# Optimization experiments

Measured on AMD Instinct MI355X. Metric: run time of the kernel, lower is better.

The kernel has to match this reference:

```python
import jax, jax.numpy as jnp
import numpy as np

EMB_SIZE = 768
NUM_HEADS = 8


def setup_inputs() -> dict:
    key = jax.random.key(0)
    ks = jax.random.split(key, 6)
    B, N, E = 8, 1024, EMB_SIZE
    return {
        "x": jax.random.normal(ks[0], (B, N, E), dtype=jnp.float32),
        "relative_pos": jax.random.normal(ks[1], (NUM_HEADS, N, N), dtype=jnp.float32),
        "qkv_w": jax.random.normal(ks[2], (2 * E, E), dtype=jnp.float32) * 0.02,
        "qkv_b": jax.random.normal(ks[3], (2 * E,), dtype=jnp.float32) * 0.02,
        "val_w": jax.random.normal(ks[4], (E, E), dtype=jnp.float32) * 0.02,
        "val_b": jax.random.normal(ks[5], (E,), dtype=jnp.float32) * 0.02,
    }


def reference(x, relative_pos, qkv_w, qkv_b, val_w, val_b):
    B, N, E = x.shape
    H = NUM_HEADS
    D = E // H
    # qkv projection: [B, N, 2E]; last dim layout is (h, d, qk) per einops rearrange
    qkv = (x @ qkv_w.T + qkv_b).reshape(B, N, H, D, 2)
    q = jnp.transpose(qkv[..., 0], (0, 2, 1, 3))  # [B, H, N, D]
    k = jnp.transpose(qkv[..., 1], (0, 2, 1, 3))  # [B, H, N, D]
    scale = E ** 0.5  # original divides by sqrt(emb_size), not sqrt(d_head)
    energy = jnp.einsum('bhqd,bhkd->bhqk', q, k) / scale  # [B, H, N, N]
    # relative_pos [H, N, N] broadcasts over batch
    energy = jax.nn.softmax(energy + relative_pos, axis=-1)
    values = x @ val_w.T + val_b  # [B, N, E]
    return values, energy
```

## Files before the change

### kernel.cpp

```cpp
#include <hip/hip_runtime.h>
#include <hip/hip_bf16.h>

#define EMB 768
#define NH 8
#define DH 96
#define BATCH 8
#define SEQ 1024
#define M_TOT (BATCH * SEQ)
#define NCOLS (3 * EMB)

typedef float f32x4 __attribute__((ext_vector_type(4)));
typedef __bf16 bf16x8 __attribute__((ext_vector_type(8)));

__device__ __forceinline__ unsigned short f2bf_bits(float f) {
  __hip_bfloat16 b = __float2bfloat16(f);
  return *reinterpret_cast<unsigned short*>(&b);
}

__device__ __forceinline__ void gload_lds16(const void* g, void* l) {
  __builtin_amdgcn_global_load_lds(
      (__attribute__((address_space(1))) void*)(g),
      (__attribute__((address_space(3))) void*)(l), 16, 0, 0);
}

__global__ void prep_x_kernel(const float* __restrict__ x, __hip_bfloat16* __restrict__ xb) {
  const int n4 = M_TOT * EMB / 4;
  int i = blockIdx.x * blockDim.x + threadIdx.x;
  if (i < n4) {
    f32x4 v = reinterpret_cast<const f32x4*>(x)[i];
    ushort4 o;
    o.x = f2bf_bits(v[0]);
    o.y = f2bf_bits(v[1]);
    o.z = f2bf_bits(v[2]);
    o.w = f2bf_bits(v[3]);
    reinterpret_cast<ushort4*>(xb)[i] = o;
  }
}

__global__ void prep_w_kernel(const float* __restrict__ qkv_w, const float* __restrict__ qkv_b,
                              const float* __restrict__ val_w, const float* __restrict__ val_b,
                              __hip_bfloat16* __restrict__ Wall, float* __restrict__ bias) {
  const float inv_s = 0.03608439182435161f;
  int idx = blockIdx.x * 256 + threadIdx.x;
  if (idx >= NCOLS * EMB) return;
  int r = idx / EMB;
  int c = idx - r * EMB;
  float v;
  if (r < EMB) {
    int h = r / DH, d = r - h * DH;
    int src = h * 192 + 2 * d;
    v = qkv_w[(size_t)src * EMB + c] * inv_s;
    if (c == 0) bias[r] = qkv_b[src] * inv_s;
  } else if (r < 2 * EMB) {
    int r2 = r - EMB;
    int h = r2 / DH, d = r2 - h * DH;
    int src = h * 192 + 2 * d + 1;
    v = qkv_w[(size_t)src * EMB + c];
    if (c == 0) bias[r] = qkv_b[src];
  } else {
    int r3 = r - 2 * EMB;
    v = val_w[(size_t)r3 * EMB + c];
    if (c == 0) bias[r] = val_b[r3];
  }
  Wall[idx] = __float2bfloat16(v);
}

__global__ __launch_bounds__(256) void gemm_kernel(
    const __hip_bfloat16* __restrict__ xb, const __hip_bfloat16* __restrict__ Wall,
    const float* __restrict__ bias, __hip_bfloat16* __restrict__ qhead,
    __hip_bfloat16* __restrict__ khead, float* __restrict__ vout) {
  __shared__ __hip_bfloat16 As[128 * 32];
  __shared__ __hip_bfloat16 Bs[128 * 32];
  const int tid = threadIdx.x;
  const int w = tid >> 6, l = tid & 63;
  const int m0 = blockIdx.x * 128;
  const int n0 = blockIdx.y * 128;
  const int wr = w >> 1, wc = w & 1;

  f32x4 acc[4][4] = {};

  const int sr0 = (w * 2 + 0) * 16 + (l >> 2);
  const int sr1 = (w * 2 + 1) * 16 + (l >> 2);
  const int sc = (l & 3) * 8;

  for (int kt = 0; kt < EMB / 32; ++kt) {
    const int k0 = kt * 32;
    gload_lds16(xb + (size_t)(m0 + sr0) * EMB + k0 + sc, (void*)(As + (w * 2 + 0) * 512));
    gload_lds16(xb + (size_t)(m0 + sr1) * EMB + k0 + sc, (void*)(As + (w * 2 + 1) * 512));
    gload_lds16(Wall + (size_t)(n0 + sr0) * EMB + k0 + sc, (void*)(Bs + (w * 2 + 0) * 512));
    gload_lds16(Wall + (size_t)(n0 + sr1) * EMB + k0 + sc, (void*)(Bs + (w * 2 + 1) * 512));
    __syncthreads();

    bf16x8 af[4], bfr[4];
#pragma unroll
    for (int t = 0; t < 4; ++t) {
      af[t] = *reinterpret_cast<const bf16x8*>(As + (wr * 64 + t * 16 + (l & 15)) * 32 + (l >> 4) * 8);
      bfr[t] = *reinterpret_cast<const bf16x8*>(Bs + (wc * 64 + t * 16 + (l & 15)) * 32 + (l >> 4) * 8);
    }
#pragma unroll
    for (int i = 0; i < 4; ++i)
#pragma unroll
      for (int j = 0; j < 4; ++j)
        acc[i][j] = __builtin_amdgcn_mfma_f32_16x16x32_bf16(af[i], bfr[j], acc[i][j], 0, 0, 0);
    __syncthreads();
  }

  const int rowbase = m0 + wr * 64;
  const int colbase = n0 + wc * 64;
#pragma unroll
  for (int j = 0; j < 4; ++j) {
    const int n = colbase + j * 16 + (l & 15);
    const float bb = bias[n];
#pragma unroll
    for (int i = 0; i < 4; ++i) {
#pragma unroll
      for (int q = 0; q < 4; ++q) {
        const int m = rowbase + i * 16 + (l >> 4) * 4 + q;
        const float v = acc[i][j][q] + bb;
        if (n0 >= 2 * EMB) {
          vout[(size_t)m * EMB + (n - 2 * EMB)] = v;
        } else {
          const int nn = (n0 >= EMB) ? (n - EMB) : n;
          const int hh = nn / DH, dd = nn - hh * DH;
          const size_t off = ((size_t)((m >> 10) * NH + hh) * SEQ + (m & 1023)) * DH + dd;
          if (n0 >= EMB) khead[off] = __float2bfloat16(v);
          else qhead[off] = __float2bfloat16(v);
        }
      }
    }
  }
}

__global__ __launch_bounds__(512, 4) void attn_kernel(
    const __hip_bfloat16* __restrict__ qhead, const __hip_bfloat16* __restrict__ khead,
    const float* __restrict__ rel, float* __restrict__ eout) {
  __shared__ alignas(16) char KS[49152];
  __shared__ float redm[16][8];
  __shared__ float reds[16][8];

  const int t = threadIdx.x;
  const int w = t >> 6, l = t & 63;
  const int lr = l >> 4, lc = l & 15;
  const int flat = blockIdx.x;
  const int u = flat >> 6;
  const int b = (flat >> 3) & 7;
  const int g = u * 8 + (flat & 7);
  const int h = g >> 6;
  const int rb = g & 63;
  const int row0 = rb * 16;

  const __hip_bfloat16* qsrc = qhead + ((size_t)(b * NH + h) * SEQ + row0 + lc) * DH;
  bf16x8 qf[3];
#pragma unroll
  for (int kc = 0; kc < 3; ++kc)
    qf[kc] = *reinterpret_cast<const bf16x8*>(qsrc + kc * 32 + lr * 8);

  const __hip_bfloat16* ksrc =
      khead + (size_t)(b * NH + h) * SEQ * DH + (size_t)w * 16 * DH;
  char* kdst = KS + w * 6144;

#define STAGE_K(c, buf)                                                             \
  {                                                                                 \
    const __hip_bfloat16* s_ = ksrc + (size_t)(c) * 12288 + (size_t)l * 8;          \
    gload_lds16(s_, kdst + (buf) * 3072);                                           \
    gload_lds16(s_ + 512, kdst + (buf) * 3072 + 1024);                              \
    gload_lds16(s_ + 1024, kdst + (buf) * 3072 + 2048);                             \
  }

  STAGE_K(0, 0)

  const float* relsrc = rel + ((size_t)h * SEQ + row0 + lc) * SEQ + w * 16 + lr * 4;
  f32x4 acc[8];

#pragma unroll
  for (int c = 0; c < 8; ++c) {
    f32x4 relv = *reinterpret_cast<const f32x4*>(relsrc + c * 128);
    if (c < 7) STAGE_K(c + 1, (c + 1) & 1)
    if (c < 7) {
      asm volatile("s_waitcnt vmcnt(4)" ::: "memory");
    } else {
      asm volatile("s_waitcnt vmcnt(1)" ::: "memory");
    }
    __builtin_amdgcn_sched_barrier(0);
    const __hip_bfloat16* kp =
        reinterpret_cast<const __hip_bfloat16*>(kdst + (c & 1) * 3072) + lc * DH;
    f32x4 a = {0.f, 0.f, 0.f, 0.f};
#pragma unroll
    for (int kc = 0; kc < 3; ++kc) {
      bf16x8 kf = *reinterpret_cast<const bf16x8*>(kp + kc * 32 + lr * 8);
      a = __builtin_amdgcn_mfma_f32_16x16x32_bf16(kf, qf[kc], a, 0, 0, 0);
    }
    acc[c] = a + relv;
  }
#undef STAGE_K

  float mx = -3.4e38f;
#pragma unroll
  for (int c = 0; c < 8; ++c)
    mx = fmaxf(mx, fmaxf(fmaxf(acc[c][0], acc[c][1]), fmaxf(acc[c][2], acc[c][3])));
  mx = fmaxf(mx, __shfl_xor(mx, 16));
  mx = fmaxf(mx, __shfl_xor(mx, 32));
  if (l < 16) redm[lc][w] = mx;
  __syncthreads();
  float M = redm[lc][0];
#pragma unroll
  for (int i = 1; i < 8; ++i) M = fmaxf(M, redm[lc][i]);

  float sm = 0.f;
#pragma unroll
  for (int c = 0; c < 8; ++c) {
#pragma unroll
    for (int j = 0; j < 4; ++j) {
      float e = __expf(acc[c][j] - M);
      acc[c][j] = e;
      sm += e;
    }
  }
  sm += __shfl_xor(sm, 16);
  sm += __shfl_xor(sm, 32);
  if (l < 16) reds[lc][w] = sm;
  __syncthreads();
  float S = 0.f;
#pragma unroll
  for (int i = 0; i < 8; ++i) S += reds[lc][i];
  const float rinv = 1.0f / S;

  float* op = eout + ((size_t)(b * NH + h) * SEQ + row0 + lc) * SEQ + w * 16 + lr * 4;
#pragma unroll
  for (int c = 0; c < 8; ++c) {
    f32x4 v = acc[c] * rinv;
    *reinterpret_cast<f32x4*>(op + c * 128) = v;
  }
}

extern "C" void kernel_launch(void* const* d_in, const int* in_sizes, int n_in,
                              void* d_out, int out_size, void* d_ws, size_t ws_size,
                              hipStream_t stream) {
  const float* x = (const float*)d_in[0];
  const float* rel = (const float*)d_in[1];
  const float* qkv_w = (const float*)d_in[2];
  const float* qkv_b = (const float*)d_in[3];
  const float* val_w = (const float*)d_in[4];
  const float* val_b = (const float*)d_in[5];
  float* out = (float*)d_out;

  char* ws = (char*)d_ws;
  __hip_bfloat16* xb = (__hip_bfloat16*)(ws);
  __hip_bfloat16* Wall = (__hip_bfloat16*)(ws + 12582912);
  float* bias = (float*)(ws + 16121856);
  __hip_bfloat16* qhead = (__hip_bfloat16*)(ws + 16131072);
  __hip_bfloat16* khead = (__hip_bfloat16*)(ws + 28713984);

  float* vout = out;
  float* eout = out + (size_t)M_TOT * EMB;

  prep_x_kernel<<<dim3(M_TOT * EMB / 4 / 256), dim3(256), 0, stream>>>(x, xb);
  prep_w_kernel<<<dim3(NCOLS * EMB / 256), dim3(256), 0, stream>>>(qkv_w, qkv_b, val_w, val_b,
                                                                   Wall, bias);
  gemm_kernel<<<dim3(M_TOT / 128, NCOLS / 128), dim3(256), 0, stream>>>(xb, Wall, bias, qhead,
                                                                        khead, vout);
  attn_kernel<<<dim3(SEQ / 16 * NH * BATCH), dim3(512), 0, stream>>>(qhead, khead, rel, eout);
}
```

Measured before the change: 197.3 us.

## Stage GEMM q/k epilogue through LDS and triple-buffer K in attention

```diff
diff --git a/kernel.cpp b/kernel.cpp
--- a/kernel.cpp
+++ b/kernel.cpp
@@ -71,6 +71,7 @@
     __hip_bfloat16* __restrict__ khead, float* __restrict__ vout) {
   __shared__ __hip_bfloat16 As[128 * 32];
   __shared__ __hip_bfloat16 Bs[128 * 32];
+  __shared__ __hip_bfloat16 Cs[128][136];
   const int tid = threadIdx.x;
   const int w = tid >> 6, l = tid & 63;
   const int m0 = blockIdx.x * 128;
@@ -105,36 +106,57 @@
     __syncthreads();
   }
 
-  const int rowbase = m0 + wr * 64;
-  const int colbase = n0 + wc * 64;
-#pragma unroll
-  for (int j = 0; j < 4; ++j) {
-    const int n = colbase + j * 16 + (l & 15);
-    const float bb = bias[n];
-#pragma unroll
-    for (int i = 0; i < 4; ++i) {
-#pragma unroll
-      for (int q = 0; q < 4; ++q) {
-        const int m = rowbase + i * 16 + (l >> 4) * 4 + q;
-        const float v = acc[i][j][q] + bb;
-        if (n0 >= 2 * EMB) {
-          vout[(size_t)m * EMB + (n - 2 * EMB)] = v;
-        } else {
-          const int nn = (n0 >= EMB) ? (n - EMB) : n;
-          const int hh = nn / DH, dd = nn - hh * DH;
-          const size_t off = ((size_t)((m >> 10) * NH + hh) * SEQ + (m & 1023)) * DH + dd;
-          if (n0 >= EMB) khead[off] = __float2bfloat16(v);
-          else qhead[off] = __float2bfloat16(v);
+  if (n0 >= 2 * EMB) {
+    const int rowbase = m0 + wr * 64;
+    const int colbase = n0 - 2 * EMB + wc * 64;
+#pragma unroll
+    for (int j = 0; j < 4; ++j) {
+      const int n = colbase + j * 16 + (l & 15);
+      const float bb = bias[2 * EMB + n];
+#pragma unroll
+      for (int i = 0; i < 4; ++i) {
+#pragma unroll
+        for (int q = 0; q < 4; ++q) {
+          const int m = rowbase + i * 16 + (l >> 4) * 4 + q;
+          vout[(size_t)m * EMB + n] = acc[i][j][q] + bb;
         }
       }
     }
-  }
-}
-
-__global__ __launch_bounds__(512, 4) void attn_kernel(
+  } else {
+#pragma unroll
+    for (int j = 0; j < 4; ++j) {
+      const int nl = wc * 64 + j * 16 + (l & 15);
+      const float bb = bias[n0 + nl];
+#pragma unroll
+      for (int i = 0; i < 4; ++i) {
+#pragma unroll
+        for (int q = 0; q < 4; ++q) {
+          const int ml = wr * 64 + i * 16 + (l >> 4) * 4 + q;
+          Cs[ml][nl] = __float2bfloat16(acc[i][j][q] + bb);
+        }
+      }
+    }
+    __syncthreads();
+    __hip_bfloat16* dst = (n0 >= EMB) ? khead : qhead;
+    const int ch0 = (n0 >= EMB) ? (n0 - EMB) : n0;
+    const int cg = (tid & 15) * 8;
+    const int gch = ch0 + cg;
+    const int hh = gch / DH, dd = gch - hh * DH;
+#pragma unroll
+    for (int pass = 0; pass < 8; ++pass) {
+      const int r = pass * 16 + (tid >> 4);
+      const int m = m0 + r;
+      const int bb_ = m >> 10, mm = m & 1023;
+      bf16x8 v8 = *reinterpret_cast<const bf16x8*>(&Cs[r][cg]);
+      *reinterpret_cast<bf16x8*>(dst + ((size_t)(bb_ * NH + hh) * SEQ + mm) * DH + dd) = v8;
+    }
+  }
+}
+
+__global__ __launch_bounds__(512, 2) void attn_kernel(
     const __hip_bfloat16* __restrict__ qhead, const __hip_bfloat16* __restrict__ khead,
     const float* __restrict__ rel, float* __restrict__ eout) {
-  __shared__ alignas(16) char KS[49152];
+  __shared__ alignas(16) char KS[8 * 3 * 3072];
   __shared__ float redm[16][8];
   __shared__ float reds[16][8];
 
@@ -155,9 +177,15 @@
   for (int kc = 0; kc < 3; ++kc)
     qf[kc] = *reinterpret_cast<const bf16x8*>(qsrc + kc * 32 + lr * 8);
 
+  const float* relsrc = rel + ((size_t)h * SEQ + row0 + lc) * SEQ + w * 16 + lr * 4;
+  f32x4 relv[8];
+#pragma unroll
+  for (int c = 0; c < 8; ++c)
+    relv[c] = *reinterpret_cast<const f32x4*>(relsrc + c * 128);
+
   const __hip_bfloat16* ksrc =
       khead + (size_t)(b * NH + h) * SEQ * DH + (size_t)w * 16 * DH;
-  char* kdst = KS + w * 6144;
+  char* kdst = KS + w * 9216;
 
 #define STAGE_K(c, buf)                                                             \
   {                                                                                 \
@@ -168,29 +196,31 @@
   }
 
   STAGE_K(0, 0)
-
-  const float* relsrc = rel + ((size_t)h * SEQ + row0 + lc) * SEQ + w * 16 + lr * 4;
+  STAGE_K(1, 1)
+
   f32x4 acc[8];
-
 #pragma unroll
   for (int c = 0; c < 8; ++c) {
-    f32x4 relv = *reinterpret_cast<const f32x4*>(relsrc + c * 128);
-    if (c < 7) STAGE_K(c + 1, (c + 1) & 1)
-    if (c < 7) {
-      asm volatile("s_waitcnt vmcnt(4)" ::: "memory");
+    if (c < 6) STAGE_K(c + 2, (c + 2) % 3)
+    if (c < 6) {
+      asm volatile("s_waitcnt vmcnt(6)" ::: "memory");
+    } else if (c == 6) {
+      asm volatile("s_waitcnt vmcnt(3)" ::: "memory");
     } else {
-      asm volatile("s_waitcnt vmcnt(1)" ::: "memory");
+      asm volatile("s_waitcnt vmcnt(0)" ::: "memory");
     }
     __builtin_amdgcn_sched_barrier(0);
     const __hip_bfloat16* kp =
-        reinterpret_cast<const __hip_bfloat16*>(kdst + (c & 1) * 3072) + lc * DH;
+        reinterpret_cast<const __hip_bfloat16*>(kdst + (c % 3) * 3072) + lc * DH;
     f32x4 a = {0.f, 0.f, 0.f, 0.f};
+    __builtin_amdgcn_s_setprio(1);
 #pragma unroll
     for (int kc = 0; kc < 3; ++kc) {
       bf16x8 kf = *reinterpret_cast<const bf16x8*>(kp + kc * 32 + lr * 8);
       a = __builtin_amdgcn_mfma_f32_16x16x32_bf16(kf, qf[kc], a, 0, 0, 0);
     }
-    acc[c] = a + relv;
+    __builtin_amdgcn_s_setprio(0);
+    acc[c] = a + relv[c];
   }
 #undef STAGE_K
 
```

Result: faster. 182.4 us (-7.5%).
